# Kernel tuning notes

Measured on AMD Instinct MI355X. Metric: run time of the kernel, lower is better.

Reference implementation:

```python
import jax, jax.numpy as jnp
import numpy as np

BATCH, SEQ, D_IN, D_HID, N_CLS = 256, 128, 1024, 2048, 1024


def setup_inputs() -> dict:
    key = jax.random.key(0)
    ks = jax.random.split(key, 6)
    s_in = 1.0 / np.sqrt(D_IN)
    s_hid = 1.0 / np.sqrt(D_HID)
    return {
        "x": jax.random.normal(ks[0], (BATCH, SEQ, D_IN), dtype=jnp.float32),
        "W_hx": jax.random.normal(ks[1], (D_HID, D_IN), dtype=jnp.float32) * s_in,
        "W_hh": jax.random.normal(ks[2], (D_HID, D_HID), dtype=jnp.float32) * s_hid,
        "W_ph": jax.random.normal(ks[3], (N_CLS, D_HID), dtype=jnp.float32) * s_hid,
        "b_h": jax.random.normal(ks[4], (D_HID,), dtype=jnp.float32) * 0.01,
        "b_p": jax.random.normal(ks[5], (N_CLS,), dtype=jnp.float32) * 0.01,
    }


def reference(x, W_hx, W_hh, W_ph, b_h, b_p):
    # Input projection for all timesteps in one large GEMM: [B,S,Din] @ [Din,H] -> [B,S,H]
    xproj = jnp.einsum("bsd,hd->bsh", x, W_hx) + b_h  # bias folded in once per step
    h0 = jnp.zeros((x.shape[0], W_hh.shape[0]), dtype=x.dtype)

    def step(h_prev, xp_t):
        # h_t = W_hx x_t + W_hh h_prev + b_h (linear recurrence, as in source)
        h_t = xp_t + h_prev @ W_hh.T
        return h_t, None

    # scan over time axis: xproj transposed to [S,B,H]
    h_T, _ = jax.lax.scan(step, h0, jnp.swapaxes(xproj, 0, 1))
    # readout from final hidden state: p = W_ph h_T + b_p -> [B, C]
    p = h_T @ W_ph.T + b_p
    return p
```

## Files before the change

kernel.cpp:

```cpp
#include <hip/hip_runtime.h>
#include <stdint.h>

#define B_SZ   256
#define SEQ_LEN 128
#define DIN    1024
#define DHID   2048
#define NCLS   1024
#define NBLK   256
#define NROUND 8

typedef unsigned short ushort_t;
typedef short bf16x8 __attribute__((ext_vector_type(8)));
typedef float f32x16 __attribute__((ext_vector_type(16)));
typedef ushort_t u16x8 __attribute__((ext_vector_type(8)));

__device__ __forceinline__ ushort_t f32_to_bf16(float f) {
  uint32_t u = __builtin_bit_cast(uint32_t, f);
  u = (u + 0x7FFFu + ((u >> 16) & 1u)) >> 16;
  return (ushort_t)u;
}
__device__ __forceinline__ float bf16_to_f32(ushort_t h) {
  uint32_t u = ((uint32_t)h) << 16;
  return __builtin_bit_cast(float, u);
}

__device__ __forceinline__ void llds16(const ushort_t* g, ushort_t* l) {
  __builtin_amdgcn_global_load_lds(
      (const __attribute__((address_space(1))) void*)g,
      (__attribute__((address_space(3))) void*)l, 16, 0, 0);
}

__device__ __forceinline__ void cstore_f32(float* p, float v) {
  __hip_atomic_store(p, v, __ATOMIC_RELAXED, __HIP_MEMORY_SCOPE_AGENT);
}
__device__ __forceinline__ void cstore_u64(void* p, uint64_t v) {
  __hip_atomic_store((uint64_t*)p, v, __ATOMIC_RELAXED, __HIP_MEMORY_SCOPE_AGENT);
}
__device__ __forceinline__ uint64_t cload_u64(const void* p) {
  return __hip_atomic_load((const uint64_t*)p, __ATOMIC_RELAXED, __HIP_MEMORY_SCOPE_AGENT);
}
__device__ __forceinline__ void cstore_u32(unsigned* p, unsigned v) {
  __hip_atomic_store(p, v, __ATOMIC_RELAXED, __HIP_MEMORY_SCOPE_AGENT);
}
__device__ __forceinline__ unsigned cload_u32(const unsigned* p) {
  return __hip_atomic_load(p, __ATOMIC_RELAXED, __HIP_MEMORY_SCOPE_AGENT);
}

__device__ __forceinline__ void gsync(unsigned* flags, unsigned ep) {
  __syncthreads();
  if (threadIdx.x == 0) cstore_u32(&flags[blockIdx.x], ep);
  if (threadIdx.x < 64) {
    const unsigned* f = flags + threadIdx.x * 4;
    for (;;) {
      unsigned a = cload_u32(f + 0), b = cload_u32(f + 1);
      unsigned c = cload_u32(f + 2), d = cload_u32(f + 3);
      bool ok = (a >= ep) & (b >= ep) & (c >= ep) & (d >= ep);
      if (__ballot(ok) == ~0ull) break;
      __builtin_amdgcn_s_sleep(1);
    }
  }
  __syncthreads();
}

__global__ void k_split(const float* __restrict__ s, ushort_t* __restrict__ hi,
                        ushort_t* __restrict__ lo, int n4) {
  int i = blockIdx.x * 256 + threadIdx.x;
  if (i >= n4) return;
  float4 v = ((const float4*)s)[i];
  ushort_t h0 = f32_to_bf16(v.x), h1 = f32_to_bf16(v.y);
  ushort_t h2 = f32_to_bf16(v.z), h3 = f32_to_bf16(v.w);
  ushort4 hv; hv.x = h0; hv.y = h1; hv.z = h2; hv.w = h3;
  ushort4 lv;
  lv.x = f32_to_bf16(v.x - bf16_to_f32(h0));
  lv.y = f32_to_bf16(v.y - bf16_to_f32(h1));
  lv.z = f32_to_bf16(v.z - bf16_to_f32(h2));
  lv.w = f32_to_bf16(v.w - bf16_to_f32(h3));
  ((ushort4*)hi)[i] = hv;
  ((ushort4*)lo)[i] = lv;
}

__global__ void k_cvt(const float* __restrict__ s, ushort_t* __restrict__ d, int n4) {
  int i = blockIdx.x * 256 + threadIdx.x;
  if (i >= n4) return;
  float4 v = ((const float4*)s)[i];
  ushort4 hv;
  hv.x = f32_to_bf16(v.x); hv.y = f32_to_bf16(v.y);
  hv.z = f32_to_bf16(v.z); hv.w = f32_to_bf16(v.w);
  ((ushort4*)d)[i] = hv;
}

__global__ void k_cvtT(const float* __restrict__ s, ushort_t* __restrict__ d) {
  int i = blockIdx.x * 256 + threadIdx.x;
  int dd = (i & (DIN / 8 - 1)) * 8;
  int bs = i >> 7;
  int b = bs >> 7;
  int t = bs & (SEQ_LEN - 1);
  const float* src = s + (size_t)bs * DIN + dd;
  float4 v0 = *(const float4*)src;
  float4 v1 = *(const float4*)(src + 4);
  u16x8 hv;
  hv[0] = f32_to_bf16(v0.x); hv[1] = f32_to_bf16(v0.y);
  hv[2] = f32_to_bf16(v0.z); hv[3] = f32_to_bf16(v0.w);
  hv[4] = f32_to_bf16(v1.x); hv[5] = f32_to_bf16(v1.y);
  hv[6] = f32_to_bf16(v1.z); hv[7] = f32_to_bf16(v1.w);
  *(u16x8*)(d + ((size_t)t * B_SZ + b) * DIN + dd) = hv;
}

__global__ void k_trb(const ushort_t* __restrict__ src, ushort_t* __restrict__ dst) {
  __shared__ ushort_t t[64][65];
  const int bx = blockIdx.x * 64, by = blockIdx.y * 64;
  const int c = threadIdx.x & 63, r0 = (threadIdx.x >> 6) * 16;
#pragma unroll
  for (int i = 0; i < 16; ++i)
    t[r0 + i][c] = src[(size_t)(by + r0 + i) * DHID + bx + c];
  __syncthreads();
#pragma unroll
  for (int i = 0; i < 16; ++i)
    dst[(size_t)(bx + r0 + i) * DHID + by + c] = t[c][r0 + i];
}

__global__ void k_trg(const ushort_t* __restrict__ src, ushort_t* __restrict__ dst,
                      int srcld, int dstld) {
  __shared__ ushort_t t[64][65];
  const int bx = blockIdx.x * 64, by = blockIdx.y * 64;
  const int c = threadIdx.x & 63, r0 = (threadIdx.x >> 6) * 16;
#pragma unroll
  for (int i = 0; i < 16; ++i)
    t[r0 + i][c] = src[(size_t)(by + r0 + i) * srcld + bx + c];
  __syncthreads();
#pragma unroll
  for (int i = 0; i < 16; ++i)
    dst[(size_t)(bx + r0 + i) * dstld + by + c] = t[c][r0 + i];
}

__global__ void k_bvec(const float* __restrict__ W, const float* __restrict__ b,
                       float* __restrict__ out) {
  int row = (blockIdx.x * blockDim.x + threadIdx.x) >> 6;
  int lane = threadIdx.x & 63;
  if (row >= DHID) return;
  float s = 0.0f;
  for (int j = lane; j < DHID; j += 64) s += W[(size_t)row * DHID + j] * b[j];
#pragma unroll
  for (int off = 32; off; off >>= 1) s += __shfl_down(s, off);
  if (lane == 0) out[row] = b[row] + s;
}

struct BigArgs {
  const ushort_t* A[3];
  const ushort_t* B[3];
  int nseg;
  int klen;
  size_t tA, sA;
  size_t ldo;
  const ushort_t* D;
  size_t tD;
  const float* bias;
  ushort_t* out_hi;
  ushort_t* out_lo;
  int lognx;
};

__device__ __forceinline__ void big_epi(const BigArgs& a, f32x16 (&acc)[2][2],
                                        int bm0, int bn0) {
  const int tid = threadIdx.x, lane = tid & 63, wv = tid >> 6;
  const int l31 = lane & 31, half = lane >> 5;
  int gm0 = bm0 + (wv & 1) * 64, gn0 = bn0 + (wv >> 1) * 64;
#pragma unroll
  for (int mi = 0; mi < 2; ++mi)
#pragma unroll
    for (int ni = 0; ni < 2; ++ni)
#pragma unroll
      for (int r = 0; r < 16; ++r) {
        int row = gm0 + mi * 32 + (r & 3) + 8 * (r >> 2) + 4 * half;
        int col = gn0 + ni * 32 + l31;
        float v = acc[mi][ni][r];
        if (a.bias) v += a.bias[col];
        if (a.D)
          v += bf16_to_f32(a.D[(size_t)(row >> 8) * a.tD +
                               (size_t)(row & 255) * 2048 + col]);
        ushort_t hh = f32_to_bf16(v);
        a.out_hi[(size_t)row * a.ldo + col] = hh;
        if (a.out_lo)
          a.out_lo[(size_t)row * a.ldo + col] = f32_to_bf16(v - bf16_to_f32(hh));
      }
}

__device__ __forceinline__ void big_body_db(const BigArgs& a, int wg) {
  __shared__ __align__(16) ushort_t lds[32768];
  const int tid = threadIdx.x, lane = tid & 63, wv = tid >> 6;
  const int l31 = lane & 31, half = lane >> 5;

  const int bn0 = (wg & ((1 << a.lognx) - 1)) * 128;
  const int bm0 = (wg >> a.lognx) * 128;
  const int t_ = bm0 >> 8, mrem = bm0 & 255;
  const int kit = a.klen >> 6;

  f32x16 acc[2][2];
#pragma unroll
  for (int p = 0; p < 2; ++p)
#pragma unroll
    for (int q = 0; q < 2; ++q)
#pragma unroll
      for (int r = 0; r < 16; ++r) acc[p][q][r] = 0.0f;

  auto stage = [&](int buf, int i) {
    int seg = 0, ii = i;
    while (ii >= kit) { ii -= kit; ++seg; }
    const int kc = ii * 64;
    const ushort_t* Ab = a.A[seg];
    const ushort_t* Bb = a.B[seg];
#pragma unroll
    for (int j = 0; j < 4; ++j) {
      int s = tid + 256 * j;
      int prow = s >> 3, glc = (s & 7) ^ (prow & 7);
      llds16(Ab + (size_t)t_ * a.tA + (size_t)(mrem + prow) * a.sA + (kc + glc * 8),
             &lds[(size_t)(buf * 16384 + (wv * 64 + 256 * j) * 16) / 2]);
      llds16(Bb + (size_t)(bn0 + prow) * a.klen + (kc + glc * 8),
             &lds[(size_t)(32768 + buf * 16384 + (wv * 64 + 256 * j) * 16) / 2]);
    }
  };

  const int nit = a.nseg * kit;
  stage(0, 0);
  for (int i = 0; i < nit; ++i) {
    int buf = i & 1;
    if (i + 1 < nit) {
      stage(buf ^ 1, i + 1);
      __builtin_amdgcn_s_waitcnt(0x3FF0 | 8);
    } else {
      __builtin_amdgcn_s_waitcnt(0x3FF0);
    }
    __builtin_amdgcn_s_barrier();
    const ushort_t* At = &lds[buf * 8192];
    const ushort_t* Bt = &lds[16384 + buf * 8192];
#pragma unroll
    for (int ks = 0; ks < 4; ++ks) {
      int ch = ks * 2 + half;
      bf16x8 af[2], bf_[2];
#pragma unroll
      for (int mi = 0; mi < 2; ++mi) {
        int row = (wv & 1) * 64 + mi * 32 + l31;
        int pch = ch ^ (row & 7);
        af[mi] = *(const bf16x8*)&At[row * 64 + pch * 8];
      }
#pragma unroll
      for (int ni = 0; ni < 2; ++ni) {
        int row = (wv >> 1) * 64 + ni * 32 + l31;
        int pch = ch ^ (row & 7);
        bf_[ni] = *(const bf16x8*)&Bt[row * 64 + pch * 8];
      }
#pragma unroll
      for (int mi = 0; mi < 2; ++mi)
#pragma unroll
        for (int ni = 0; ni < 2; ++ni)
          acc[mi][ni] = __builtin_amdgcn_mfma_f32_32x32x16_bf16(
              af[mi], bf_[ni], acc[mi][ni], 0, 0, 0);
    }
    __builtin_amdgcn_s_barrier();
  }
  big_epi(a, acc, bm0, bn0);
}

__device__ __forceinline__ void big_body_sb(const BigArgs& a, int wg) {
  __shared__ __align__(16) ushort_t lds[16384];
  const int tid = threadIdx.x, lane = tid & 63, wv = tid >> 6;
  const int l31 = lane & 31, half = lane >> 5;

  const int bn0 = (wg & ((1 << a.lognx) - 1)) * 128;
  const int bm0 = (wg >> a.lognx) * 128;
  const int t_ = bm0 >> 8, mrem = bm0 & 255;
  const int kit = a.klen >> 6;

  f32x16 acc[2][2];
#pragma unroll
  for (int p = 0; p < 2; ++p)
#pragma unroll
    for (int q = 0; q < 2; ++q)
#pragma unroll
      for (int r = 0; r < 16; ++r) acc[p][q][r] = 0.0f;

  auto stage = [&](int i) {
    int seg = 0, ii = i;
    while (ii >= kit) { ii -= kit; ++seg; }
    const int kc = ii * 64;
    const ushort_t* Ab = a.A[seg];
    const ushort_t* Bb = a.B[seg];
#pragma unroll
    for (int j = 0; j < 4; ++j) {
      int s = tid + 256 * j;
      int prow = s >> 3, glc = (s & 7) ^ (prow & 7);
      llds16(Ab + (size_t)t_ * a.tA + (size_t)(mrem + prow) * a.sA + (kc + glc * 8),
             &lds[(size_t)((wv * 64 + 256 * j) * 16) / 2]);
      llds16(Bb + (size_t)(bn0 + prow) * a.klen + (kc + glc * 8),
             &lds[(size_t)(16384 + (wv * 64 + 256 * j) * 16) / 2]);
    }
  };

  const int nit = a.nseg * kit;
  for (int i = 0; i < nit; ++i) {
    stage(i);
    __builtin_amdgcn_s_waitcnt(0x3FF0);
    __builtin_amdgcn_s_barrier();
    const ushort_t* At = &lds[0];
    const ushort_t* Bt = &lds[8192];
#pragma unroll
    for (int ks = 0; ks < 4; ++ks) {
      int ch = ks * 2 + half;
      bf16x8 af[2], bf_[2];
#pragma unroll
      for (int mi = 0; mi < 2; ++mi) {
        int row = (wv & 1) * 64 + mi * 32 + l31;
        int pch = ch ^ (row & 7);
        af[mi] = *(const bf16x8*)&At[row * 64 + pch * 8];
      }
#pragma unroll
      for (int ni = 0; ni < 2; ++ni) {
        int row = (wv >> 1) * 64 + ni * 32 + l31;
        int pch = ch ^ (row & 7);
        bf_[ni] = *(const bf16x8*)&Bt[row * 64 + pch * 8];
      }
#pragma unroll
      for (int mi = 0; mi < 2; ++mi)
#pragma unroll
        for (int ni = 0; ni < 2; ++ni)
          acc[mi][ni] = __builtin_amdgcn_mfma_f32_32x32x16_bf16(
              af[mi], bf_[ni], acc[mi][ni], 0, 0, 0);
    }
    __builtin_amdgcn_s_barrier();
  }
  big_epi(a, acc, bm0, bn0);
}

__global__ __launch_bounds__(256, 1) void k_big2(BigArgs a0, BigArgs a1, int nblk0) {
  int wg = blockIdx.x;
  if (wg < nblk0) {
    big_body_db(a0, wg);
  } else {
    big_body_db(a1, wg - nblk0);
  }
}

__global__ __launch_bounds__(256, 4) void k_big1s(BigArgs a) {
  big_body_sb(a, blockIdx.x);
}
__global__ __launch_bounds__(256, 4) void k_big2s(BigArgs a0, BigArgs a1, int nblk0) {
  int wg = blockIdx.x;
  if (wg < nblk0) {
    big_body_sb(a0, wg);
  } else {
    big_body_sb(a1, wg - nblk0);
  }
}

__global__ __launch_bounds__(512, 2) void k_rnn(
    const ushort_t* __restrict__ w_hi, const ushort_t* __restrict__ w_lo,
    ushort_t* __restrict__ h_hi, ushort_t* __restrict__ h_lo,
    const ushort_t* __restrict__ z_hi, const ushort_t* __restrict__ z_lo,
    float* __restrict__ P, unsigned* __restrict__ flags) {
  __shared__ __align__(16) ushort_t lds[81920];
  char* ldsb = (char*)&lds[0];

  const int tid = threadIdx.x, lane = tid & 63, wv = tid >> 6;
  const int l31 = lane & 31, half = lane >> 5;
  const int kslice = wv & 1, mq = (wv >> 1) & 1, nq = wv >> 2;
  const int b = blockIdx.x;
  const int kb = b & 7, nb = (b >> 3) & 15, mb = b >> 7;
  const int n0 = nb * 128, k0 = kb * 256, m0 = mb * 128;

#pragma unroll
  for (int hl = 0; hl < 2; ++hl) {
    const ushort_t* W = hl ? w_lo : w_hi;
    for (int p = 0; p < 4; ++p)
#pragma unroll
      for (int j = 0; j < 2; ++j) {
        int s = tid + 512 * j;
        int prow = s >> 3, glc = (s & 7) ^ (prow & 7);
        const ushort_t* g = W + (size_t)(n0 + prow) * DHID + (k0 + p * 64 + glc * 8);
        ushort_t* d = (ushort_t*)(ldsb + hl * 65536 + p * 16384 + (wv * 64 + 512 * j) * 16);
        llds16(g, d);
      }
  }
  __builtin_amdgcn_s_waitcnt(0x3FF0);
  __syncthreads();

  const int srow0 = wv * 16 + (lane >> 4);
  const int skk   = 4 * (lane & 15);
  const int sg    = (lane & 15) >> 1;
  const int ssub  = lane & 1;

  uint64_t R[4][4];

  auto regload = [&](int slot, int c) {
    const ushort_t* src = (c < 4) ? h_hi : h_lo;
    const int p = c & 3;
#pragma unroll
    for (int i = 0; i < 4; ++i)
      R[slot][i] = cload_u64(src + (size_t)(m0 + srow0 + 4 * i) * DHID +
                             (k0 + p * 64 + skk));
  };
  auto dswrite = [&](int buf, int slot) {
#pragma unroll
    for (int i = 0; i < 4; ++i) {
      int lr = srow0 + 4 * i;
      *(uint64_t*)(ldsb + 131072 + buf * 16384 + lr * 128 +
                   ((sg ^ (lr & 7)) * 16) + ssub * 8) = R[slot][i];
    }
  };

  auto phaseB = [&](ushort4 zq, ushort4 zl, bool withP) {
    const int r = b;
    const int c0 = tid * 4;
    float v[4] = {bf16_to_f32(zq.x) + bf16_to_f32(zl.x),
                  bf16_to_f32(zq.y) + bf16_to_f32(zl.y),
                  bf16_to_f32(zq.z) + bf16_to_f32(zl.z),
                  bf16_to_f32(zq.w) + bf16_to_f32(zl.w)};
    if (withP) {
#pragma unroll
      for (int k = 0; k < 8; ++k) {
        const float* pp = P + ((size_t)k * B_SZ + r) * DHID + c0;
#pragma unroll
        for (int j = 0; j < 2; ++j) {
          uint64_t q = cload_u64((const uint64_t*)pp + j);
          float2 f = __builtin_bit_cast(float2, q);
          v[2 * j]     += f.x;
          v[2 * j + 1] += f.y;
        }
      }
    }
    ushort_t hh[4], ll[4];
#pragma unroll
    for (int e = 0; e < 4; ++e) {
      hh[e] = f32_to_bf16(v[e]);
      ll[e] = f32_to_bf16(v[e] - bf16_to_f32(hh[e]));
    }
    uint64_t q0, q1;
    __builtin_memcpy(&q0, &hh[0], 8);
    __builtin_memcpy(&q1, &ll[0], 8);
    cstore_u64(h_hi + (size_t)r * DHID + c0, q0);
    cstore_u64(h_lo + (size_t)r * DHID + c0, q1);
  };

  unsigned ep = 1;
  {
    ushort4 zq = *(const ushort4*)(z_hi + (size_t)b * DHID + tid * 4);
    ushort4 zl = *(const ushort4*)(z_lo + (size_t)b * DHID + tid * 4);
    phaseB(zq, zl, false);
  }
  gsync(flags, ep); ++ep;

  for (int j = 1; j < NROUND; ++j) {
    f32x16 acc[2][2];
#pragma unroll
    for (int p = 0; p < 2; ++p)
#pragma unroll
      for (int q = 0; q < 2; ++q)
#pragma unroll
        for (int r = 0; r < 16; ++r) acc[p][q][r] = 0.0f;

    regload(0, 0); regload(1, 1); regload(2, 2); regload(3, 3);
    dswrite(0, 0);
    __syncthreads();

    for (int c = 0; c < 8; ++c) {
      if (c + 4 <= 7) regload(c & 3, c + 4);
      if (c + 1 <= 7) dswrite((c + 1) & 1, (c + 1) & 3);

      const char* At = ldsb + 131072 + (c & 1) * 16384;
      const char* Bh = ldsb + (size_t)(c & 3) * 16384;
      const char* Bl = ldsb + 65536 + (size_t)(c & 3) * 16384;
      const bool isHi = c < 4;
#pragma unroll
      for (int ks = 0; ks < 2; ++ks) {
        const int g = (kslice * 2 + ks) * 2 + half;
        bf16x8 af[2], bh_[2], bl_[2];
#pragma unroll
        for (int mi = 0; mi < 2; ++mi) {
          int row = mq * 64 + mi * 32 + l31;
          af[mi] = *(const bf16x8*)(At + row * 128 + (g ^ (row & 7)) * 16);
        }
#pragma unroll
        for (int ni = 0; ni < 2; ++ni) {
          int row = nq * 64 + ni * 32 + l31;
          int off = row * 128 + (g ^ (row & 7)) * 16;
          bh_[ni] = *(const bf16x8*)(Bh + off);
          if (isHi) bl_[ni] = *(const bf16x8*)(Bl + off);
        }
#pragma unroll
        for (int mi = 0; mi < 2; ++mi)
#pragma unroll
          for (int ni = 0; ni < 2; ++ni) {
            acc[mi][ni] = __builtin_amdgcn_mfma_f32_32x32x16_bf16(
                af[mi], bh_[ni], acc[mi][ni], 0, 0, 0);
            if (isHi)
              acc[mi][ni] = __builtin_amdgcn_mfma_f32_32x32x16_bf16(
                  af[mi], bl_[ni], acc[mi][ni], 0, 0, 0);
          }
      }
      __syncthreads();
    }

    {
      float* scr = (float*)(ldsb + 131072);
      const int pr = mq * 2 + nq;
#pragma unroll
      for (int r = 0; r < 2; ++r) {
        if (kslice == 1) {
#pragma unroll
          for (int ni = 0; ni < 2; ++ni)
#pragma unroll
            for (int reg = 0; reg < 16; ++reg) {
              int row32 = (reg & 3) + 8 * (reg >> 2) + 4 * half;
              scr[pr * 2048 + row32 * 64 + ni * 32 + l31] = acc[r][ni][reg];
            }
        }
        __syncthreads();
        if (kslice == 0) {
#pragma unroll
          for (int ni = 0; ni < 2; ++ni)
#pragma unroll
            for (int reg = 0; reg < 16; ++reg) {
              int row32 = (reg & 3) + 8 * (reg >> 2) + 4 * half;
              acc[r][ni][reg] += scr[pr * 2048 + row32 * 64 + ni * 32 + l31];
            }
        }
        __syncthreads();
      }
    }

    if (kslice == 0) {
      float* Pt = P + (size_t)kb * (B_SZ * DHID);
#pragma unroll
      for (int mi = 0; mi < 2; ++mi)
#pragma unroll
        for (int ni = 0; ni < 2; ++ni)
#pragma unroll
          for (int reg = 0; reg < 16; ++reg) {
            int row = m0 + mq * 64 + mi * 32 + (reg & 3) + 8 * (reg >> 2) + 4 * half;
            int col = n0 + nq * 64 + ni * 32 + l31;
            cstore_f32(&Pt[(size_t)row * DHID + col], acc[mi][ni][reg]);
          }
    }
    ushort4 zq = *(const ushort4*)(z_hi + ((size_t)j * 256 + b) * DHID + tid * 4);
    ushort4 zl = *(const ushort4*)(z_lo + ((size_t)j * 256 + b) * DHID + tid * 4);
    gsync(flags, ep); ++ep;

    phaseB(zq, zl, true);
    gsync(flags, ep); ++ep;
  }
}

struct Seg {
  const ushort_t* A;
  const ushort_t* B;
  int a_stride;
  int b_stride;
  int k_len;
};
struct Args {
  Seg seg[4];
  int n_seg;
  int n_iters;
  const float* bias;
  ushort_t* out_hi;
  ushort_t* out_lo;
  float* out_f32;
  int ldo;
};

#define DEPTH 6
__global__ __launch_bounds__(256, 1) void k_gemm(Args args) {
  __shared__ __align__(16) char pool[DEPTH * 12288];
  const int tid = threadIdx.x, lane = tid & 63, wv = tid >> 6;
  const int bm0 = blockIdx.y * 32, bn0 = blockIdx.x * 64;

  f32x16 acc[2];
#pragma unroll
  for (int c = 0; c < 2; ++c)
#pragma unroll
    for (int r = 0; r < 16; ++r) acc[c][r] = 0.0f;

  const int prow0 = tid >> 3;
  const int glc0 = (tid & 7) ^ (prow0 & 7);
  const int prow1 = (tid + 256) >> 3;
  const int glc1 = (tid & 7) ^ (prow1 & 7);

  auto stage = [&](int buf, const Seg& sg, int k0) {
    const ushort_t* ga = sg.A + (size_t)(bm0 + prow0) * sg.a_stride + (k0 + glc0 * 8);
    const ushort_t* gb0 = sg.B + (size_t)(bn0 + prow0) * sg.b_stride + (k0 + glc0 * 8);
    const ushort_t* gb1 = sg.B + (size_t)(bn0 + prow1) * sg.b_stride + (k0 + glc1 * 8);
    ushort_t* la = (ushort_t*)(pool + buf * 12288) + wv * 512;
    ushort_t* lb = (ushort_t*)(pool + buf * 12288 + 4096) + wv * 512;
    llds16(ga, la);
    llds16(gb0, lb);
    llds16(gb1, lb + 2048);
  };

  const int nit = args.n_iters;
  int sc = 0, kc = 0;
  int nst = nit < (DEPTH - 1) ? nit : (DEPTH - 1);
  for (int s = 0; s < nst; ++s) {
    stage(s, args.seg[sc], kc);
    kc += 64;
    if (kc >= args.seg[sc].k_len) { kc = 0; ++sc; }
  }

  const int half = lane >> 5, l31 = lane & 31;
  const int lch = wv * 2 + half;
  int sb = DEPTH - 1, cb = 0;

  for (int i = 0; i < nit; ++i) {
    int ahead = nit - 1 - i;
    if (ahead > DEPTH - 1) ahead = DEPTH - 1;
    if (i + DEPTH - 1 < nit) {
      stage(sb, args.seg[sc], kc);
      if (++sb == DEPTH) sb = 0;
      kc += 64;
      if (kc >= args.seg[sc].k_len) { kc = 0; ++sc; }
    }
    switch (ahead) {
      case 5: __builtin_amdgcn_s_waitcnt(0x3FF0 | 15); break;
      case 4: __builtin_amdgcn_s_waitcnt(0x3FF0 | 12); break;
      case 3: __builtin_amdgcn_s_waitcnt(0x3FF0 | 9); break;
      case 2: __builtin_amdgcn_s_waitcnt(0x3FF0 | 6); break;
      case 1: __builtin_amdgcn_s_waitcnt(0x3FF0 | 3); break;
      default: __builtin_amdgcn_s_waitcnt(0x3FF0 | 0); break;
    }
    __builtin_amdgcn_s_barrier();

    const ushort_t* tA = (const ushort_t*)(pool + cb * 12288);
    const ushort_t* tB = tA + 2048;
    bf16x8 af, bfm[2];
    {
      int row = l31;
      int pch = lch ^ (row & 7);
      af = *(const bf16x8*)&tA[row * 64 + pch * 8];
    }
#pragma unroll
    for (int ni = 0; ni < 2; ++ni) {
      int row = ni * 32 + l31;
      int pch = lch ^ (row & 7);
      bfm[ni] = *(const bf16x8*)&tB[row * 64 + pch * 8];
    }
#pragma unroll
    for (int ni = 0; ni < 2; ++ni)
      acc[ni] = __builtin_amdgcn_mfma_f32_32x32x16_bf16(af, bfm[ni], acc[ni], 0, 0, 0);

    if (++cb == DEPTH) cb = 0;
    __builtin_amdgcn_s_barrier();
  }

  __syncthreads();
  float* red = (float*)pool + wv * 2048;
#pragma unroll
  for (int ni = 0; ni < 2; ++ni)
#pragma unroll
    for (int r = 0; r < 16; ++r) {
      int row = (r & 3) + 8 * (r >> 2) + 4 * half;
      int col = ni * 32 + l31;
      red[row * 64 + col] = acc[ni][r];
    }
  __syncthreads();

  const float* r0 = (const float*)pool;
  const float* r1 = r0 + 2048;
  const float* r2 = r0 + 4096;
  const float* r3 = r0 + 6144;
#pragma unroll
  for (int j = 0; j < 8; ++j) {
    int e = j * 256 + tid;
    int row = e >> 6, col = e & 63;
    float v = r0[e] + r1[e] + r2[e] + r3[e] + args.bias[bn0 + col];
    size_t o = (size_t)(bm0 + row) * args.ldo + (bn0 + col);
    if (args.out_f32) {
      args.out_f32[o] = v;
    } else {
      ushort_t h = f32_to_bf16(v);
      args.out_hi[o] = h;
      args.out_lo[o] = f32_to_bf16(v - bf16_to_f32(h));
    }
  }
}

extern "C" void kernel_launch(void* const* d_in, const int* in_sizes, int n_in,
                              void* d_out, int out_size, void* d_ws, size_t ws_size,
                              hipStream_t stream) {
  const float* x   = (const float*)d_in[0];
  const float* Whx = (const float*)d_in[1];
  const float* Whh = (const float*)d_in[2];
  const float* Wph = (const float*)d_in[3];
  const float* bh  = (const float*)d_in[4];
  const float* bp  = (const float*)d_in[5];

  const size_t WSZ = (size_t)DHID * DHID * 2;
  char* p = (char*)d_ws;
  ushort_t* whh_hi = (ushort_t*)p; p += WSZ;
  ushort_t* whh_lo = (ushort_t*)p; p += WSZ;
  ushort_t* whhT_hi= (ushort_t*)p; p += WSZ;
  ushort_t* whhT_lo= (ushort_t*)p; p += WSZ;
  ushort_t* w2_hi  = (ushort_t*)p; p += WSZ;
  ushort_t* w2_lo  = (ushort_t*)p; p += WSZ;
  ushort_t* w4_hi  = (ushort_t*)p; p += WSZ;
  ushort_t* w4_lo  = (ushort_t*)p; p += WSZ;
  ushort_t* w8_hi  = (ushort_t*)p; p += WSZ;
  ushort_t* w8_lo  = (ushort_t*)p; p += WSZ;
  ushort_t* w16_hi = (ushort_t*)p; p += WSZ;
  ushort_t* w16_lo = (ushort_t*)p; p += WSZ;
  ushort_t* wT_hi  = (ushort_t*)p; p += WSZ;
  ushort_t* wT_lo  = (ushort_t*)p; p += WSZ;
  ushort_t* whx_b  = (ushort_t*)p; p += (size_t)DHID * DIN * 2;
  ushort_t* whxT   = (ushort_t*)p; p += (size_t)DIN * DHID * 2;
  ushort_t* wa_b   = (ushort_t*)p; p += (size_t)DHID * DIN * 2;
  ushort_t* wph_b  = (ushort_t*)p; p += (size_t)NCLS * DHID * 2;
  ushort_t* xT     = (ushort_t*)p; p += (size_t)B_SZ * SEQ_LEN * DIN * 2;
  ushort_t* z2_b   = (ushort_t*)p; p += (size_t)64 * B_SZ * DHID * 2;
  ushort_t* z4_b   = (ushort_t*)p; p += (size_t)32 * B_SZ * DHID * 2;
  ushort_t* z8_b   = (ushort_t*)p; p += (size_t)16 * B_SZ * DHID * 2;
  ushort_t* z8_lo  = (ushort_t*)p; p += (size_t)16 * B_SZ * DHID * 2;
  ushort_t* z16_b  = (ushort_t*)p; p += (size_t)8 * B_SZ * DHID * 2;
  ushort_t* z16_lo = (ushort_t*)p; p += (size_t)8 * B_SZ * DHID * 2;
  float*    Part   = (float*)p;    p += (size_t)8 * B_SZ * DHID * 4;
  ushort_t* h_hi   = (ushort_t*)p; p += (size_t)B_SZ * DHID * 2;
  ushort_t* h_lo   = (ushort_t*)p; p += (size_t)B_SZ * DHID * 2;
  float*    b2_ws  = (float*)p;    p += (size_t)DHID * 4;
  unsigned* flags  = (unsigned*)p; p += NBLK * 4;

  hipMemsetAsync(flags, 0, NBLK * 4, stream);

  {
    int n4 = DHID * DHID / 4;
    k_split<<<(n4 + 255) / 256, 256, 0, stream>>>(Whh, whh_hi, whh_lo, n4);
  }
  k_trb<<<dim3(32, 32), 256, 0, stream>>>(whh_hi, whhT_hi);
  k_trb<<<dim3(32, 32), 256, 0, stream>>>(whh_lo, whhT_lo);
  {
    int n4 = DHID * DIN / 4;
    k_cvt<<<(n4 + 255) / 256, 256, 0, stream>>>(Whx, whx_b, n4);
  }
  {
    int n4 = NCLS * DHID / 4;
    k_cvt<<<(n4 + 255) / 256, 256, 0, stream>>>(Wph, wph_b, n4);
  }
  k_cvtT<<<(B_SZ * SEQ_LEN * DIN / 8) / 256, 256, 0, stream>>>(x, xT);
  k_trg<<<dim3(DIN / 64, DHID / 64), 256, 0, stream>>>(whx_b, whxT, DIN, DHID);
  k_bvec<<<512, 256, 0, stream>>>(Whh, bh, b2_ws);

  const size_t TBLK = (size_t)512 * DHID;

  BigArgs aWa = {};
  aWa.A[0] = whh_hi; aWa.B[0] = whxT;
  aWa.A[1] = whh_lo; aWa.B[1] = whxT;
  aWa.nseg = 2; aWa.klen = DHID; aWa.tA = (size_t)256 * DHID; aWa.sA = DHID;
  aWa.ldo = DIN; aWa.out_hi = wa_b; aWa.lognx = 3;

  BigArgs aW2 = {};
  aW2.A[0] = whh_hi; aW2.B[0] = whhT_hi;
  aW2.A[1] = whh_hi; aW2.B[1] = whhT_lo;
  aW2.A[2] = whh_lo; aW2.B[2] = whhT_hi;
  aW2.nseg = 3; aW2.klen = DHID; aW2.tA = (size_t)256 * DHID; aW2.sA = DHID;
  aW2.ldo = 2048; aW2.out_hi = w2_hi; aW2.out_lo = w2_lo; aW2.lognx = 4;

  BigArgs az2 = {};
  az2.A[0] = xT;              az2.B[0] = wa_b;
  az2.A[1] = xT + (size_t)B_SZ * DIN; az2.B[1] = whx_b;
  az2.nseg = 2; az2.klen = DIN;
  az2.tA = (size_t)2 * B_SZ * DIN; az2.sA = DIN;
  az2.ldo = 2048; az2.bias = b2_ws; az2.out_hi = z2_b; az2.lognx = 4;

  BigArgs aW4 = {};
  aW4.A[0] = w2_hi; aW4.B[0] = wT_hi;
  aW4.A[1] = w2_hi; aW4.B[1] = wT_lo;
  aW4.A[2] = w2_lo; aW4.B[2] = wT_hi;
  aW4.nseg = 3; aW4.klen = DHID; aW4.tA = (size_t)256 * DHID; aW4.sA = DHID;
  aW4.ldo = 2048; aW4.out_hi = w4_hi; aW4.out_lo = w4_lo; aW4.lognx = 4;

  BigArgs az4 = {};
  az4.A[0] = z2_b; az4.B[0] = w2_hi; az4.nseg = 1; az4.klen = DHID;
  az4.tA = TBLK; az4.sA = DHID;
  az4.D = z2_b + (size_t)256 * DHID; az4.tD = TBLK;
  az4.ldo = 2048; az4.out_hi = z4_b; az4.lognx = 4;

  BigArgs aW8 = {};
  aW8.A[0] = w4_hi; aW8.B[0] = wT_hi;
  aW8.A[1] = w4_hi; aW8.B[1] = wT_lo;
  aW8.A[2] = w4_lo; aW8.B[2] = wT_hi;
  aW8.nseg = 3; aW8.klen = DHID; aW8.tA = (size_t)256 * DHID; aW8.sA = DHID;
  aW8.ldo = 2048; aW8.out_hi = w8_hi; aW8.out_lo = w8_lo; aW8.lognx = 4;

  BigArgs az8 = {};
  az8.A[0] = z4_b; az8.B[0] = w4_hi; az8.nseg = 1; az8.klen = DHID;
  az8.tA = TBLK; az8.sA = DHID;
  az8.D = z4_b + (size_t)256 * DHID; az8.tD = TBLK;
  az8.ldo = 2048; az8.out_hi = z8_b; az8.out_lo = z8_lo; az8.lognx = 4;

  BigArgs aW16 = {};
  aW16.A[0] = w8_hi; aW16.B[0] = wT_hi;
  aW16.A[1] = w8_hi; aW16.B[1] = wT_lo;
  aW16.A[2] = w8_lo; aW16.B[2] = wT_hi;
  aW16.nseg = 3; aW16.klen = DHID; aW16.tA = (size_t)256 * DHID; aW16.sA = DHID;
  aW16.ldo = 2048; aW16.out_hi = w16_hi; aW16.out_lo = w16_lo; aW16.lognx = 4;

  BigArgs az16 = {};
  az16.A[0] = z8_b;  az16.B[0] = w8_hi;
  az16.A[1] = z8_b;  az16.B[1] = w8_lo;
  az16.A[2] = z8_lo; az16.B[2] = w8_hi;
  az16.nseg = 3; az16.klen = DHID; az16.tA = TBLK; az16.sA = DHID;
  az16.D = z8_b + (size_t)256 * DHID; az16.tD = TBLK;
  az16.ldo = 2048; az16.out_hi = z16_b; az16.out_lo = z16_lo; az16.lognx = 4;

  k_big2<<<dim3(384), 256, 0, stream>>>(aW2, aWa, 256);
  k_big1s<<<dim3(2048), 256, 0, stream>>>(az2);
  k_trb<<<dim3(32, 32), 256, 0, stream>>>(w2_hi, wT_hi);
  k_trb<<<dim3(32, 32), 256, 0, stream>>>(w2_lo, wT_lo);
  k_big2s<<<dim3(1280), 256, 0, stream>>>(aW4, az4, 256);
  k_trb<<<dim3(32, 32), 256, 0, stream>>>(w4_hi, wT_hi);
  k_trb<<<dim3(32, 32), 256, 0, stream>>>(w4_lo, wT_lo);
  k_big2s<<<dim3(768), 256, 0, stream>>>(aW8, az8, 256);
  k_trb<<<dim3(32, 32), 256, 0, stream>>>(w8_hi, wT_hi);
  k_trb<<<dim3(32, 32), 256, 0, stream>>>(w8_lo, wT_lo);
  k_big2<<<dim3(512), 256, 0, stream>>>(aW16, az16, 256);

  k_rnn<<<dim3(NBLK), 512, 0, stream>>>(w16_hi, w16_lo, h_hi, h_lo,
                                        z16_b, z16_lo, Part, flags);

  {
    Args a = {};
    a.seg[0] = { h_hi, wph_b, DHID, DHID, DHID };
    a.seg[1] = { h_lo, wph_b, DHID, DHID, DHID };
    a.n_seg = 2; a.n_iters = 2 * DHID / 64;
    a.bias = bp; a.out_hi = nullptr; a.out_lo = nullptr;
    a.out_f32 = (float*)d_out; a.ldo = NCLS;
    k_gemm<<<dim3(NCLS / 64, B_SZ / 32), 256, 0, stream>>>(a);
  }
}
```

Measured before the change: 1.002 ms.

## Fuse weight transposes into GEMM epilogues and conversion kernels

Each W-power GEMM now also writes the transposed hi/lo bf16 results through an LDS staging pass in its epilogue, which removes the separate transpose kernels between stages. The fp32-to-bf16 split and convert kernels for W_hh and W_hx now write both the normal and the transposed layout in one pass. This cuts about ten small kernel launches and the extra global-memory round trips they made. In exchange the epilogue gets heavier (extra barriers, LDS reuse after the main loop, strided 16-byte stores) and the workspace needs more buffers.

```diff
diff --git a/kernel.cpp b/kernel.cpp
--- a/kernel.cpp
+++ b/kernel.cpp
@@ -62,21 +62,49 @@
   __syncthreads();
 }
 
-__global__ void k_split(const float* __restrict__ s, ushort_t* __restrict__ hi,
-                        ushort_t* __restrict__ lo, int n4) {
-  int i = blockIdx.x * 256 + threadIdx.x;
-  if (i >= n4) return;
-  float4 v = ((const float4*)s)[i];
-  ushort_t h0 = f32_to_bf16(v.x), h1 = f32_to_bf16(v.y);
-  ushort_t h2 = f32_to_bf16(v.z), h3 = f32_to_bf16(v.w);
-  ushort4 hv; hv.x = h0; hv.y = h1; hv.z = h2; hv.w = h3;
-  ushort4 lv;
-  lv.x = f32_to_bf16(v.x - bf16_to_f32(h0));
-  lv.y = f32_to_bf16(v.y - bf16_to_f32(h1));
-  lv.z = f32_to_bf16(v.z - bf16_to_f32(h2));
-  lv.w = f32_to_bf16(v.w - bf16_to_f32(h3));
-  ((ushort4*)hi)[i] = hv;
-  ((ushort4*)lo)[i] = lv;
+__global__ void k_splitT(const float* __restrict__ src, ushort_t* __restrict__ hi,
+                         ushort_t* __restrict__ lo, ushort_t* __restrict__ hiT,
+                         ushort_t* __restrict__ loT) {
+  __shared__ ushort_t th[64][65];
+  __shared__ ushort_t tl[64][65];
+  const int bx = blockIdx.x * 64, by = blockIdx.y * 64;
+  const int c = threadIdx.x & 63, r0 = (threadIdx.x >> 6) * 16;
+#pragma unroll
+  for (int i = 0; i < 16; ++i) {
+    size_t o = (size_t)(by + r0 + i) * DHID + bx + c;
+    float v = src[o];
+    ushort_t hh = f32_to_bf16(v);
+    ushort_t ll = f32_to_bf16(v - bf16_to_f32(hh));
+    hi[o] = hh;
+    lo[o] = ll;
+    th[r0 + i][c] = hh;
+    tl[r0 + i][c] = ll;
+  }
+  __syncthreads();
+#pragma unroll
+  for (int i = 0; i < 16; ++i) {
+    size_t o = (size_t)(bx + r0 + i) * DHID + by + c;
+    hiT[o] = th[c][r0 + i];
+    loT[o] = tl[c][r0 + i];
+  }
+}
+
+__global__ void k_cvtW(const float* __restrict__ src, ushort_t* __restrict__ d,
+                       ushort_t* __restrict__ dT) {
+  __shared__ ushort_t t[64][65];
+  const int bx = blockIdx.x * 64, by = blockIdx.y * 64;
+  const int c = threadIdx.x & 63, r0 = (threadIdx.x >> 6) * 16;
+#pragma unroll
+  for (int i = 0; i < 16; ++i) {
+    size_t o = (size_t)(by + r0 + i) * DIN + bx + c;
+    ushort_t hh = f32_to_bf16(src[o]);
+    d[o] = hh;
+    t[r0 + i][c] = hh;
+  }
+  __syncthreads();
+#pragma unroll
+  for (int i = 0; i < 16; ++i)
+    dT[(size_t)(bx + r0 + i) * DHID + by + c] = t[c][r0 + i];
 }
 
 __global__ void k_cvt(const float* __restrict__ s, ushort_t* __restrict__ d, int n4) {
@@ -106,33 +134,6 @@
   *(u16x8*)(d + ((size_t)t * B_SZ + b) * DIN + dd) = hv;
 }
 
-__global__ void k_trb(const ushort_t* __restrict__ src, ushort_t* __restrict__ dst) {
-  __shared__ ushort_t t[64][65];
-  const int bx = blockIdx.x * 64, by = blockIdx.y * 64;
-  const int c = threadIdx.x & 63, r0 = (threadIdx.x >> 6) * 16;
-#pragma unroll
-  for (int i = 0; i < 16; ++i)
-    t[r0 + i][c] = src[(size_t)(by + r0 + i) * DHID + bx + c];
-  __syncthreads();
-#pragma unroll
-  for (int i = 0; i < 16; ++i)
-    dst[(size_t)(bx + r0 + i) * DHID + by + c] = t[c][r0 + i];
-}
-
-__global__ void k_trg(const ushort_t* __restrict__ src, ushort_t* __restrict__ dst,
-                      int srcld, int dstld) {
-  __shared__ ushort_t t[64][65];
-  const int bx = blockIdx.x * 64, by = blockIdx.y * 64;
-  const int c = threadIdx.x & 63, r0 = (threadIdx.x >> 6) * 16;
-#pragma unroll
-  for (int i = 0; i < 16; ++i)
-    t[r0 + i][c] = src[(size_t)(by + r0 + i) * srcld + bx + c];
-  __syncthreads();
-#pragma unroll
-  for (int i = 0; i < 16; ++i)
-    dst[(size_t)(bx + r0 + i) * dstld + by + c] = t[c][r0 + i];
-}
-
 __global__ void k_bvec(const float* __restrict__ W, const float* __restrict__ b,
                        float* __restrict__ out) {
   int row = (blockIdx.x * blockDim.x + threadIdx.x) >> 6;
@@ -157,11 +158,13 @@
   const float* bias;
   ushort_t* out_hi;
   ushort_t* out_lo;
+  ushort_t* out_hiT;
+  ushort_t* out_loT;
   int lognx;
 };
 
 __device__ __forceinline__ void big_epi(const BigArgs& a, f32x16 (&acc)[2][2],
-                                        int bm0, int bn0) {
+                                        int bm0, int bn0, char* ldsb) {
   const int tid = threadIdx.x, lane = tid & 63, wv = tid >> 6;
   const int l31 = lane & 31, half = lane >> 5;
   int gm0 = bm0 + (wv & 1) * 64, gn0 = bn0 + (wv >> 1) * 64;
@@ -183,6 +186,43 @@
         if (a.out_lo)
           a.out_lo[(size_t)row * a.ldo + col] = f32_to_bf16(v - bf16_to_f32(hh));
       }
+
+  if (a.out_hiT) {
+    float* scr = (float*)ldsb;
+    const int nT = tid >> 1;
+    const int mT0 = (tid & 1) * 32;
+#pragma unroll
+    for (int pp = 0; pp < 2; ++pp) {
+      __syncthreads();
+      if ((wv & 1) == pp) {
+#pragma unroll
+        for (int mi = 0; mi < 2; ++mi)
+#pragma unroll
+          for (int ni = 0; ni < 2; ++ni)
+#pragma unroll
+            for (int r = 0; r < 16; ++r) {
+              int lr = mi * 32 + (r & 3) + 8 * (r >> 2) + 4 * half;
+              int bc = (wv >> 1) * 64 + ni * 32 + l31;
+              scr[lr * 128 + bc] = acc[mi][ni][r];
+            }
+      }
+      __syncthreads();
+      size_t o = (size_t)(bn0 + nT) * a.ldo + bm0 + pp * 64 + mT0;
+#pragma unroll
+      for (int j = 0; j < 4; ++j) {
+        u16x8 hv, lv;
+#pragma unroll
+        for (int i = 0; i < 8; ++i) {
+          float v = scr[(mT0 + j * 8 + i) * 128 + nT];
+          ushort_t hh = f32_to_bf16(v);
+          hv[i] = hh;
+          lv[i] = f32_to_bf16(v - bf16_to_f32(hh));
+        }
+        *(u16x8*)(a.out_hiT + o + j * 8) = hv;
+        *(u16x8*)(a.out_loT + o + j * 8) = lv;
+      }
+    }
+  }
 }
 
 __device__ __forceinline__ void big_body_db(const BigArgs& a, int wg) {
@@ -258,7 +298,7 @@
     }
     __builtin_amdgcn_s_barrier();
   }
-  big_epi(a, acc, bm0, bn0);
+  big_epi(a, acc, bm0, bn0, (char*)&lds[0]);
 }
 
 __device__ __forceinline__ void big_body_sb(const BigArgs& a, int wg) {
@@ -328,7 +368,7 @@
     }
     __builtin_amdgcn_s_barrier();
   }
-  big_epi(a, acc, bm0, bn0);
+  big_epi(a, acc, bm0, bn0, (char*)&lds[0]);
 }
 
 __global__ __launch_bounds__(256, 1) void k_big2(BigArgs a0, BigArgs a1, int nblk0) {
@@ -699,14 +739,18 @@
   ushort_t* whhT_lo= (ushort_t*)p; p += WSZ;
   ushort_t* w2_hi  = (ushort_t*)p; p += WSZ;
   ushort_t* w2_lo  = (ushort_t*)p; p += WSZ;
+  ushort_t* w2T_hi = (ushort_t*)p; p += WSZ;
+  ushort_t* w2T_lo = (ushort_t*)p; p += WSZ;
   ushort_t* w4_hi  = (ushort_t*)p; p += WSZ;
   ushort_t* w4_lo  = (ushort_t*)p; p += WSZ;
+  ushort_t* w4T_hi = (ushort_t*)p; p += WSZ;
+  ushort_t* w4T_lo = (ushort_t*)p; p += WSZ;
   ushort_t* w8_hi  = (ushort_t*)p; p += WSZ;
   ushort_t* w8_lo  = (ushort_t*)p; p += WSZ;
+  ushort_t* w8T_hi = (ushort_t*)p; p += WSZ;
+  ushort_t* w8T_lo = (ushort_t*)p; p += WSZ;
   ushort_t* w16_hi = (ushort_t*)p; p += WSZ;
   ushort_t* w16_lo = (ushort_t*)p; p += WSZ;
-  ushort_t* wT_hi  = (ushort_t*)p; p += WSZ;
-  ushort_t* wT_lo  = (ushort_t*)p; p += WSZ;
   ushort_t* whx_b  = (ushort_t*)p; p += (size_t)DHID * DIN * 2;
   ushort_t* whxT   = (ushort_t*)p; p += (size_t)DIN * DHID * 2;
   ushort_t* wa_b   = (ushort_t*)p; p += (size_t)DHID * DIN * 2;
@@ -726,22 +770,13 @@
 
   hipMemsetAsync(flags, 0, NBLK * 4, stream);
 
-  {
-    int n4 = DHID * DHID / 4;
-    k_split<<<(n4 + 255) / 256, 256, 0, stream>>>(Whh, whh_hi, whh_lo, n4);
-  }
-  k_trb<<<dim3(32, 32), 256, 0, stream>>>(whh_hi, whhT_hi);
-  k_trb<<<dim3(32, 32), 256, 0, stream>>>(whh_lo, whhT_lo);
-  {
-    int n4 = DHID * DIN / 4;
-    k_cvt<<<(n4 + 255) / 256, 256, 0, stream>>>(Whx, whx_b, n4);
-  }
+  k_splitT<<<dim3(32, 32), 256, 0, stream>>>(Whh, whh_hi, whh_lo, whhT_hi, whhT_lo);
   {
     int n4 = NCLS * DHID / 4;
     k_cvt<<<(n4 + 255) / 256, 256, 0, stream>>>(Wph, wph_b, n4);
   }
   k_cvtT<<<(B_SZ * SEQ_LEN * DIN / 8) / 256, 256, 0, stream>>>(x, xT);
-  k_trg<<<dim3(DIN / 64, DHID / 64), 256, 0, stream>>>(whx_b, whxT, DIN, DHID);
+  k_cvtW<<<dim3(DIN / 64, DHID / 64), 256, 0, stream>>>(Whx, whx_b, whxT);
   k_bvec<<<512, 256, 0, stream>>>(Whh, bh, b2_ws);
 
   const size_t TBLK = (size_t)512 * DHID;
@@ -757,7 +792,8 @@
   aW2.A[1] = whh_hi; aW2.B[1] = whhT_lo;
   aW2.A[2] = whh_lo; aW2.B[2] = whhT_hi;
   aW2.nseg = 3; aW2.klen = DHID; aW2.tA = (size_t)256 * DHID; aW2.sA = DHID;
-  aW2.ldo = 2048; aW2.out_hi = w2_hi; aW2.out_lo = w2_lo; aW2.lognx = 4;
+  aW2.ldo = 2048; aW2.out_hi = w2_hi; aW2.out_lo = w2_lo;
+  aW2.out_hiT = w2T_hi; aW2.out_loT = w2T_lo; aW2.lognx = 4;
 
   BigArgs az2 = {};
   az2.A[0] = xT;              az2.B[0] = wa_b;
@@ -767,11 +803,12 @@
   az2.ldo = 2048; az2.bias = b2_ws; az2.out_hi = z2_b; az2.lognx = 4;
 
   BigArgs aW4 = {};
-  aW4.A[0] = w2_hi; aW4.B[0] = wT_hi;
-  aW4.A[1] = w2_hi; aW4.B[1] = wT_lo;
-  aW4.A[2] = w2_lo; aW4.B[2] = wT_hi;
+  aW4.A[0] = w2_hi; aW4.B[0] = w2T_hi;
+  aW4.A[1] = w2_hi; aW4.B[1] = w2T_lo;
+  aW4.A[2] = w2_lo; aW4.B[2] = w2T_hi;
   aW4.nseg = 3; aW4.klen = DHID; aW4.tA = (size_t)256 * DHID; aW4.sA = DHID;
-  aW4.ldo = 2048; aW4.out_hi = w4_hi; aW4.out_lo = w4_lo; aW4.lognx = 4;
+  aW4.ldo = 2048; aW4.out_hi = w4_hi; aW4.out_lo = w4_lo;
+  aW4.out_hiT = w4T_hi; aW4.out_loT = w4T_lo; aW4.lognx = 4;
 
   BigArgs az4 = {};
   az4.A[0] = z2_b; az4.B[0] = w2_hi; az4.nseg = 1; az4.klen = DHID;
@@ -780,11 +817,12 @@
   az4.ldo = 2048; az4.out_hi = z4_b; az4.lognx = 4;
 
   BigArgs aW8 = {};
-  aW8.A[0] = w4_hi; aW8.B[0] = wT_hi;
-  aW8.A[1] = w4_hi; aW8.B[1] = wT_lo;
-  aW8.A[2] = w4_lo; aW8.B[2] = wT_hi;
+  aW8.A[0] = w4_hi; aW8.B[0] = w4T_hi;
+  aW8.A[1] = w4_hi; aW8.B[1] = w4T_lo;
+  aW8.A[2] = w4_lo; aW8.B[2] = w4T_hi;
   aW8.nseg = 3; aW8.klen = DHID; aW8.tA = (size_t)256 * DHID; aW8.sA = DHID;
-  aW8.ldo = 2048; aW8.out_hi = w8_hi; aW8.out_lo = w8_lo; aW8.lognx = 4;
+  aW8.ldo = 2048; aW8.out_hi = w8_hi; aW8.out_lo = w8_lo;
+  aW8.out_hiT = w8T_hi; aW8.out_loT = w8T_lo; aW8.lognx = 4;
 
   BigArgs az8 = {};
   az8.A[0] = z4_b; az8.B[0] = w4_hi; az8.nseg = 1; az8.klen = DHID;
@@ -793,9 +831,9 @@
   az8.ldo = 2048; az8.out_hi = z8_b; az8.out_lo = z8_lo; az8.lognx = 4;
 
   BigArgs aW16 = {};
-  aW16.A[0] = w8_hi; aW16.B[0] = wT_hi;
-  aW16.A[1] = w8_hi; aW16.B[1] = wT_lo;
-  aW16.A[2] = w8_lo; aW16.B[2] = wT_hi;
+  aW16.A[0] = w8_hi; aW16.B[0] = w8T_hi;
+  aW16.A[1] = w8_hi; aW16.B[1] = w8T_lo;
+  aW16.A[2] = w8_lo; aW16.B[2] = w8T_hi;
   aW16.nseg = 3; aW16.klen = DHID; aW16.tA = (size_t)256 * DHID; aW16.sA = DHID;
   aW16.ldo = 2048; aW16.out_hi = w16_hi; aW16.out_lo = w16_lo; aW16.lognx = 4;
 
@@ -809,14 +847,8 @@
 
   k_big2<<<dim3(384), 256, 0, stream>>>(aW2, aWa, 256);
   k_big1s<<<dim3(2048), 256, 0, stream>>>(az2);
-  k_trb<<<dim3(32, 32), 256, 0, stream>>>(w2_hi, wT_hi);
-  k_trb<<<dim3(32, 32), 256, 0, stream>>>(w2_lo, wT_lo);
   k_big2s<<<dim3(1280), 256, 0, stream>>>(aW4, az4, 256);
-  k_trb<<<dim3(32, 32), 256, 0, stream>>>(w4_hi, wT_hi);
-  k_trb<<<dim3(32, 32), 256, 0, stream>>>(w4_lo, wT_lo);
   k_big2s<<<dim3(768), 256, 0, stream>>>(aW8, az8, 256);
-  k_trb<<<dim3(32, 32), 256, 0, stream>>>(w8_hi, wT_hi);
-  k_trb<<<dim3(32, 32), 256, 0, stream>>>(w8_lo, wT_lo);
   k_big2<<<dim3(512), 256, 0, stream>>>(aW16, az16, 256);
 
   k_rnn<<<dim3(NBLK), 512, 0, stream>>>(w16_hi, w16_lo, h_hi, h_lo,
```

After: 1.033 ms. 3.1% more time.
